# Performance work log

Measured on AMD Instinct MI355X. Metric: run time of the kernel, lower is better.

Reference implementation:

```python
import jax, jax.numpy as jnp
import numpy as np

PAD = 0  # padding_idx


def setup_inputs() -> dict:
    key = jax.random.key(0)
    ks = jax.random.split(key, 10)
    T, B, V, E, H = 64, 32, 32000, 512, 512
    s = 0.05
    tokens = jax.random.randint(ks[0], (T, B), 0, V).astype(jnp.int32)
    emb = jax.random.normal(ks[1], (V, E), jnp.float32) * s
    emb = emb.at[PAD].set(0.0)  # padding_idx row zeroed like nn.Embedding
    return {
        "tokens": tokens,
        "emb": emb,
        "W_ih": jax.random.normal(ks[2], (4 * H, E), jnp.float32) * s,
        "W_hh": jax.random.normal(ks[3], (4 * H, H), jnp.float32) * s,
        "b_ih": jax.random.normal(ks[4], (4 * H,), jnp.float32) * s,
        "b_hh": jax.random.normal(ks[5], (4 * H,), jnp.float32) * s,
        "W_fc": jax.random.normal(ks[6], (V, H), jnp.float32) * s,
        "b_fc": jax.random.normal(ks[7], (V,), jnp.float32) * s,
        "h0": jax.random.normal(ks[8], (B, H), jnp.float32) * s,
        "c0": jax.random.normal(ks[9], (B, H), jnp.float32) * s,
    }


def reference(tokens, emb, W_ih, W_hh, b_ih, b_hh, W_fc, b_fc, h0, c0):
    H = h0.shape[1]

    def step(carry, tok):
        h, c = carry                      # [B,H] each
        x = emb[tok]                      # [B,E] per-token embedding lookup
        gates = x @ W_ih.T + h @ W_hh.T + b_ih + b_hh  # [B,4H]
        i, f, g, o = jnp.split(gates, 4, axis=-1)
        i = jax.nn.sigmoid(i)
        f = jax.nn.sigmoid(f)
        g = jnp.tanh(g)
        o = jax.nn.sigmoid(o)
        c_tmp = f * c + i * g             # LSTMCell cell update
        h_tmp = o * jnp.tanh(c_tmp)
        mask = (tok != PAD)[:, None]      # masked state update: carry state only for non-pad tokens
        h_new = jnp.where(mask, h_tmp, h)
        c_new = jnp.where(mask, c_tmp, c)
        logits = h_tmp @ W_fc.T + b_fc    # [B,V] projection of the tentative hidden (as in source)
        return (h_new, c_new), logits

    (_, _), out = jax.lax.scan(step, (h0, c0), tokens)  # out: [T,B,V]
    return out
```

## Files before the change

### kernel.cpp

```cpp
#include <hip/hip_runtime.h>
#include <stdint.h>

#define TT 64
#define BB 32
#define VV 32000
#define EE 512
#define HH 512
#define G4 2048
#define NBLK 64

typedef float f32x4 __attribute__((ext_vector_type(4)));
typedef short bf16x8 __attribute__((ext_vector_type(8)));

__device__ __forceinline__ unsigned int f2bf(float f) {
    union { float f; uint32_t u; } v; v.f = f;
    uint32_t r = v.u + 0x7fffu + ((v.u >> 16) & 1u);
    return (r >> 16);
}

__global__ __launch_bounds__(256)
void prep_kernel(const float* __restrict__ emb, const int* __restrict__ tokens,
                 const float* __restrict__ h0,
                 unsigned short* __restrict__ Xbf, unsigned short* __restrict__ hb0,
                 unsigned int* __restrict__ syncp) {
    const int NX = TT * BB * EE / 4;
    const int NH = BB * HH / 4;
    int i = blockIdx.x * 256 + threadIdx.x;
    if (i == 0) { syncp[0] = 0u; }
    if (i < NX) {
        int rrow = i >> 7;
        int e4 = i & 127;
        int tok = tokens[rrow];
        float4 v = ((const float4*)(emb + (size_t)tok * EE))[e4];
        uint2 o;
        o.x = f2bf(v.x) | (f2bf(v.y) << 16);
        o.y = f2bf(v.z) | (f2bf(v.w) << 16);
        *(uint2*)(Xbf + (size_t)rrow * EE + e4 * 4) = o;
        return;
    }
    i -= NX;
    if (i < NH) {
        float4 v = ((const float4*)h0)[i];
        uint2 o;
        o.x = f2bf(v.x) | (f2bf(v.y) << 16);
        o.y = f2bf(v.z) | (f2bf(v.w) << 16);
        *(uint2*)(hb0 + i * 4) = o;
    }
}

#define LDA 68

__global__ __launch_bounds__(256, 2)
void gemm_bt(const unsigned short* __restrict__ A, const float* __restrict__ Bm,
             float* __restrict__ Cout, const float* __restrict__ bias1,
             const float* __restrict__ bias2, int N, int K) {
    __shared__ unsigned short lA[128 * LDA];
    __shared__ unsigned short lB[128 * LDA];
    const int tid = threadIdx.x;
    const int lane = tid & 63;
    const int w = tid >> 6;
    const int m0 = blockIdx.y * 128;
    const int n0 = blockIdx.x * 128;
    const int wm = (w & 1) * 64;
    const int wn = (w >> 1) * 64;
    f32x4 acc[4][4];
#pragma unroll
    for (int i = 0; i < 4; ++i)
#pragma unroll
        for (int j = 0; j < 4; ++j) acc[i][j] = (f32x4){0.f, 0.f, 0.f, 0.f};

    for (int k0 = 0; k0 < K; k0 += 64) {
#pragma unroll
        for (int i = 0; i < 4; ++i) {
            int c = tid + 256 * i;
            int row = c >> 3;
            int kg = c & 7;
            uint4 va = *(const uint4*)(A + (size_t)(m0 + row) * K + k0 + kg * 8);
            *(uint2*)&lA[row * LDA + kg * 8]     = make_uint2(va.x, va.y);
            *(uint2*)&lA[row * LDA + kg * 8 + 4] = make_uint2(va.z, va.w);
            const float4* bp = (const float4*)(Bm + (size_t)(n0 + row) * K + k0 + kg * 8);
            float4 b0 = bp[0], b1 = bp[1];
            uint2 p0, p1;
            p0.x = f2bf(b0.x) | (f2bf(b0.y) << 16);
            p0.y = f2bf(b0.z) | (f2bf(b0.w) << 16);
            p1.x = f2bf(b1.x) | (f2bf(b1.y) << 16);
            p1.y = f2bf(b1.z) | (f2bf(b1.w) << 16);
            *(uint2*)&lB[row * LDA + kg * 8]     = p0;
            *(uint2*)&lB[row * LDA + kg * 8 + 4] = p1;
        }
        __syncthreads();
#pragma unroll
        for (int ks = 0; ks < 2; ++ks) {
            const int kgrp = ks * 4 + (lane >> 4);
            bf16x8 af[4], bfr[4];
#pragma unroll
            for (int mi = 0; mi < 4; ++mi) {
                int row = wm + mi * 16 + (lane & 15);
                union { uint2 d[2]; bf16x8 v; } u;
                u.d[0] = *(const uint2*)&lA[row * LDA + kgrp * 8];
                u.d[1] = *(const uint2*)&lA[row * LDA + kgrp * 8 + 4];
                af[mi] = u.v;
            }
#pragma unroll
            for (int ni = 0; ni < 4; ++ni) {
                int row = wn + ni * 16 + (lane & 15);
                union { uint2 d[2]; bf16x8 v; } u;
                u.d[0] = *(const uint2*)&lB[row * LDA + kgrp * 8];
                u.d[1] = *(const uint2*)&lB[row * LDA + kgrp * 8 + 4];
                bfr[ni] = u.v;
            }
#pragma unroll
            for (int mi = 0; mi < 4; ++mi)
#pragma unroll
                for (int ni = 0; ni < 4; ++ni)
                    acc[mi][ni] = __builtin_amdgcn_mfma_f32_16x16x32_bf16(
                        af[mi], bfr[ni], acc[mi][ni], 0, 0, 0);
        }
        __syncthreads();
    }
    const int col_l = lane & 15;
    const int row_l = (lane >> 4) * 4;
#pragma unroll
    for (int ni = 0; ni < 4; ++ni) {
        int col = n0 + wn + ni * 16 + col_l;
        float bv = bias1[col];
        if (bias2) bv += bias2[col];
#pragma unroll
        for (int mi = 0; mi < 4; ++mi) {
            int rowb = m0 + wm + mi * 16 + row_l;
#pragma unroll
            for (int rr = 0; rr < 4; ++rr) {
                Cout[(size_t)(rowb + rr) * N + col] = acc[mi][ni][rr] + bv;
            }
        }
    }
}

__global__ __launch_bounds__(256, 1)
void rec_kernel(const float* __restrict__ XG, const float* __restrict__ Whh,
                const int* __restrict__ tokens, const float* __restrict__ h0,
                const float* __restrict__ c0, unsigned short* __restrict__ hb0,
                unsigned short* __restrict__ hb1, unsigned short* __restrict__ Htmp,
                unsigned int* __restrict__ syncp) {
    __shared__ int ltok[TT * BB];
    const int tid = threadIdx.x;
    const int l = tid & 63;
    const int w = tid >> 6;
    const int mi = w >> 1;
    const int ni = w & 1;
    const int blk = blockIdx.x;

    for (int u = tid; u < TT * BB; u += 256) ltok[u] = tokens[u];

    const int b  = ni * 16 + (l & 15);
    const int hc = mi * 4 + (l >> 4);
    const int jh = blk * 8 + hc;

    const int r = mi * 16 + (l & 15);
    const int hcr = r >> 2;
    const int gr = r & 3;
    const int ksub = (l >> 4) * 8;
    const float* wrow = Whh + ((size_t)gr * HH + (size_t)blk * 8 + hcr) * HH;
    bf16x8 af[16];
#pragma unroll
    for (int kc = 0; kc < 16; ++kc) {
        float4 w0 = *(const float4*)(wrow + kc * 32 + ksub);
        float4 w1 = *(const float4*)(wrow + kc * 32 + ksub + 4);
        union { unsigned short s[8]; bf16x8 v; } u;
        u.s[0] = (unsigned short)f2bf(w0.x);
        u.s[1] = (unsigned short)f2bf(w0.y);
        u.s[2] = (unsigned short)f2bf(w0.z);
        u.s[3] = (unsigned short)f2bf(w0.w);
        u.s[4] = (unsigned short)f2bf(w1.x);
        u.s[5] = (unsigned short)f2bf(w1.y);
        u.s[6] = (unsigned short)f2bf(w1.z);
        u.s[7] = (unsigned short)f2bf(w1.w);
        af[kc] = u.v;
    }

    float hprev = h0[(size_t)b * HH + jh];
    float cprev = c0[(size_t)b * HH + jh];
    __syncthreads();

    for (int t = 0; t < TT; ++t) {
        const unsigned short* hin = (t & 1) ? hb1 : hb0;
        unsigned short* hout = (t & 1) ? hb0 : hb1;

        const float* xg = XG + ((size_t)t * BB + b) * G4 + jh;
        float x0 = xg[0];
        float x1 = xg[HH];
        float x2 = xg[2 * HH];
        float x3 = xg[3 * HH];

        const unsigned short* hrow = hin + (size_t)b * HH + ksub;
        f32x4 acc = {0.f, 0.f, 0.f, 0.f};
#pragma unroll
        for (int kc = 0; kc < 16; ++kc) {
            bf16x8 bfv = *(const bf16x8*)(hrow + kc * 32);
            acc = __builtin_amdgcn_mfma_f32_16x16x32_bf16(af[kc], bfv, acc, 0, 0, 0);
        }

        float gi = acc[0] + x0;
        float gf = acc[1] + x1;
        float gg = acc[2] + x2;
        float go = acc[3] + x3;
        float ig = 1.f / (1.f + __expf(-gi));
        float fg = 1.f / (1.f + __expf(-gf));
        float gt = tanhf(gg);
        float og = 1.f / (1.f + __expf(-go));
        float c_tmp = fg * cprev + ig * gt;
        float h_tmp = og * tanhf(c_tmp);
        const bool msk = ltok[t * BB + b] != 0;
        cprev = msk ? c_tmp : cprev;
        hprev = msk ? h_tmp : hprev;

        Htmp[((size_t)t * BB + b) * HH + jh] = (unsigned short)f2bf(h_tmp);
        hout[(size_t)b * HH + jh] = (unsigned short)f2bf(hprev);

        if (t < TT - 1) {
            __syncthreads();
            if (tid == 0) {
                __hip_atomic_fetch_add(syncp, 1u, __ATOMIC_RELEASE,
                                       __HIP_MEMORY_SCOPE_AGENT);
                const unsigned int tgt = (unsigned int)(t + 1) * NBLK;
                while (__hip_atomic_load(syncp, __ATOMIC_RELAXED,
                                         __HIP_MEMORY_SCOPE_AGENT) < tgt) {
                    __builtin_amdgcn_s_sleep(2);
                }
                (void)__hip_atomic_load(syncp, __ATOMIC_ACQUIRE,
                                        __HIP_MEMORY_SCOPE_AGENT);
            }
            __syncthreads();
        }
    }
}

extern "C" void kernel_launch(void* const* d_in, const int* in_sizes, int n_in,
                              void* d_out, int out_size, void* d_ws, size_t ws_size,
                              hipStream_t stream) {
    const int*   tokens = (const int*)d_in[0];
    const float* emb    = (const float*)d_in[1];
    const float* W_ih   = (const float*)d_in[2];
    const float* W_hh   = (const float*)d_in[3];
    const float* b_ih   = (const float*)d_in[4];
    const float* b_hh   = (const float*)d_in[5];
    const float* W_fc   = (const float*)d_in[6];
    const float* b_fc   = (const float*)d_in[7];
    const float* h0     = (const float*)d_in[8];
    const float* c0     = (const float*)d_in[9];

    char* ws = (char*)d_ws;
    size_t o = 0;
    unsigned short* Xbf  = (unsigned short*)(ws + o); o += (size_t)TT * BB * EE * 2;
    unsigned short* Htmp = (unsigned short*)(ws + o); o += (size_t)TT * BB * HH * 2;
    float* XG = (float*)(ws + o); o += (size_t)TT * BB * G4 * 4;
    unsigned short* hb0 = (unsigned short*)(ws + o); o += (size_t)BB * HH * 2;
    unsigned short* hb1 = (unsigned short*)(ws + o); o += (size_t)BB * HH * 2;
    unsigned int* syncp = (unsigned int*)(ws + o); o += 64;
    (void)ws_size; (void)in_sizes; (void)n_in; (void)out_size;

    prep_kernel<<<1040, 256, 0, stream>>>(emb, tokens, h0, Xbf, hb0, syncp);
    dim3 gx(G4 / 128, (TT * BB) / 128);
    gemm_bt<<<gx, 256, 0, stream>>>(Xbf, W_ih, XG, b_ih, b_hh, G4, EE);
    rec_kernel<<<NBLK, 256, 0, stream>>>(XG, W_hh, tokens, h0, c0, hb0, hb1,
                                         Htmp, syncp);
    dim3 gp(VV / 128, (TT * BB) / 128);
    gemm_bt<<<gp, 256, 0, stream>>>(Htmp, W_fc, (float*)d_out, b_fc, nullptr, VV, HH);
}
```

Measured before the change: 947.8 us.

## Pre-convert weights to bf16, use LDS DMA loads, flag barrier, interleaved gate layout

Weight conversion to bf16 for W_ih and W_fc moves into the prep kernel, so the GEMM can stage A and B tiles straight into LDS with global_load_lds instead of converting in the inner loop. GEMM blocks are remapped with an XCD-aware swizzle. The input-gate GEMM writes its output with the four gates interleaved, so the recurrence reads one float4 per step and prefetches the next step's value. The single atomic-counter grid barrier becomes a flag-and-broadcast barrier coordinated by block 0. The cost is an extra bf16 copy of the 32000x512 W_fc and an unpadded LDS layout that may cause bank conflicts.

```diff
diff --git a/kernel.cpp b/kernel.cpp
--- a/kernel.cpp
+++ b/kernel.cpp
@@ -17,50 +17,80 @@
     uint32_t r = v.u + 0x7fffu + ((v.u >> 16) & 1u);
     return (r >> 16);
 }
+__device__ __forceinline__ uint2 pack4(float4 v) {
+    uint2 o;
+    o.x = f2bf(v.x) | (f2bf(v.y) << 16);
+    o.y = f2bf(v.z) | (f2bf(v.w) << 16);
+    return o;
+}
+
+__device__ __forceinline__ void gload16(const unsigned short* g, unsigned short* l) {
+    __builtin_amdgcn_global_load_lds(
+        (const __attribute__((address_space(1))) unsigned int*)g,
+        (__attribute__((address_space(3))) unsigned int*)l, 16, 0, 0);
+}
 
 __global__ __launch_bounds__(256)
 void prep_kernel(const float* __restrict__ emb, const int* __restrict__ tokens,
-                 const float* __restrict__ h0,
+                 const float* __restrict__ h0, const float* __restrict__ Wih,
+                 const float* __restrict__ Wfc,
                  unsigned short* __restrict__ Xbf, unsigned short* __restrict__ hb0,
+                 unsigned short* __restrict__ Wib, unsigned short* __restrict__ Wfb,
                  unsigned int* __restrict__ syncp) {
     const int NX = TT * BB * EE / 4;
     const int NH = BB * HH / 4;
-    int i = blockIdx.x * 256 + threadIdx.x;
-    if (i == 0) { syncp[0] = 0u; }
-    if (i < NX) {
-        int rrow = i >> 7;
-        int e4 = i & 127;
-        int tok = tokens[rrow];
-        float4 v = ((const float4*)(emb + (size_t)tok * EE))[e4];
-        uint2 o;
-        o.x = f2bf(v.x) | (f2bf(v.y) << 16);
-        o.y = f2bf(v.z) | (f2bf(v.w) << 16);
-        *(uint2*)(Xbf + (size_t)rrow * EE + e4 * 4) = o;
-        return;
-    }
-    i -= NX;
-    if (i < NH) {
-        float4 v = ((const float4*)h0)[i];
-        uint2 o;
-        o.x = f2bf(v.x) | (f2bf(v.y) << 16);
-        o.y = f2bf(v.z) | (f2bf(v.w) << 16);
-        *(uint2*)(hb0 + i * 4) = o;
-    }
-}
-
-#define LDA 68
+    const int NWI = G4 * EE / 4;
+    const int NWF = VV * HH / 4;
+    const int NS = NBLK * 16 + 16;
+    const long total = (long)NX + NH + NWI + NWF + NS;
+    for (long idx = (long)blockIdx.x * 256 + threadIdx.x; idx < total;
+         idx += (long)gridDim.x * 256) {
+        long i = idx;
+        if (i < NX) {
+            int rrow = (int)(i >> 7);
+            int e4 = (int)(i & 127);
+            int tok = tokens[rrow];
+            float4 v = ((const float4*)(emb + (size_t)tok * EE))[e4];
+            *(uint2*)(Xbf + (size_t)rrow * EE + e4 * 4) = pack4(v);
+            continue;
+        }
+        i -= NX;
+        if (i < NH) {
+            float4 v = ((const float4*)h0)[i];
+            *(uint2*)(hb0 + i * 4) = pack4(v);
+            continue;
+        }
+        i -= NH;
+        if (i < NWI) {
+            float4 v = ((const float4*)Wih)[i];
+            *(uint2*)(Wib + i * 4) = pack4(v);
+            continue;
+        }
+        i -= NWI;
+        if (i < NWF) {
+            float4 v = ((const float4*)Wfc)[i];
+            *(uint2*)(Wfb + i * 4) = pack4(v);
+            continue;
+        }
+        i -= NWF;
+        syncp[i] = 0u;
+    }
+}
 
 __global__ __launch_bounds__(256, 2)
-void gemm_bt(const unsigned short* __restrict__ A, const float* __restrict__ Bm,
+void gemm_bb(const unsigned short* __restrict__ A, const unsigned short* __restrict__ B,
              float* __restrict__ Cout, const float* __restrict__ bias1,
-             const float* __restrict__ bias2, int N, int K) {
-    __shared__ unsigned short lA[128 * LDA];
-    __shared__ unsigned short lB[128 * LDA];
+             const float* __restrict__ bias2, int N, int K, int ntn, int mode) {
+    __shared__ unsigned short lA[128 * 64];
+    __shared__ unsigned short lB[128 * 64];
     const int tid = threadIdx.x;
     const int lane = tid & 63;
     const int w = tid >> 6;
-    const int m0 = blockIdx.y * 128;
-    const int n0 = blockIdx.x * 128;
+    const int nwg = gridDim.x;
+    const int cpx = nwg >> 3;
+    const int wid = (blockIdx.x & 7) * cpx + (blockIdx.x >> 3);
+    const int m0 = (wid / ntn) * 128;
+    const int n0 = (wid % ntn) * 128;
     const int wm = (w & 1) * 64;
     const int wn = (w >> 1) * 64;
     f32x4 acc[4][4];
@@ -72,21 +102,11 @@
     for (int k0 = 0; k0 < K; k0 += 64) {
 #pragma unroll
         for (int i = 0; i < 4; ++i) {
-            int c = tid + 256 * i;
+            int c = i * 256 + tid;
             int row = c >> 3;
             int kg = c & 7;
-            uint4 va = *(const uint4*)(A + (size_t)(m0 + row) * K + k0 + kg * 8);
-            *(uint2*)&lA[row * LDA + kg * 8]     = make_uint2(va.x, va.y);
-            *(uint2*)&lA[row * LDA + kg * 8 + 4] = make_uint2(va.z, va.w);
-            const float4* bp = (const float4*)(Bm + (size_t)(n0 + row) * K + k0 + kg * 8);
-            float4 b0 = bp[0], b1 = bp[1];
-            uint2 p0, p1;
-            p0.x = f2bf(b0.x) | (f2bf(b0.y) << 16);
-            p0.y = f2bf(b0.z) | (f2bf(b0.w) << 16);
-            p1.x = f2bf(b1.x) | (f2bf(b1.y) << 16);
-            p1.y = f2bf(b1.z) | (f2bf(b1.w) << 16);
-            *(uint2*)&lB[row * LDA + kg * 8]     = p0;
-            *(uint2*)&lB[row * LDA + kg * 8 + 4] = p1;
+            gload16(A + (size_t)(m0 + row) * K + k0 + kg * 8, &lA[c * 8]);
+            gload16(B + (size_t)(n0 + row) * K + k0 + kg * 8, &lB[c * 8]);
         }
         __syncthreads();
 #pragma unroll
@@ -96,18 +116,12 @@
 #pragma unroll
             for (int mi = 0; mi < 4; ++mi) {
                 int row = wm + mi * 16 + (lane & 15);
-                union { uint2 d[2]; bf16x8 v; } u;
-                u.d[0] = *(const uint2*)&lA[row * LDA + kgrp * 8];
-                u.d[1] = *(const uint2*)&lA[row * LDA + kgrp * 8 + 4];
-                af[mi] = u.v;
+                af[mi] = *(const bf16x8*)&lA[row * 64 + kgrp * 8];
             }
 #pragma unroll
             for (int ni = 0; ni < 4; ++ni) {
                 int row = wn + ni * 16 + (lane & 15);
-                union { uint2 d[2]; bf16x8 v; } u;
-                u.d[0] = *(const uint2*)&lB[row * LDA + kgrp * 8];
-                u.d[1] = *(const uint2*)&lB[row * LDA + kgrp * 8 + 4];
-                bfr[ni] = u.v;
+                bfr[ni] = *(const bf16x8*)&lB[row * 64 + kgrp * 8];
             }
 #pragma unroll
             for (int mi = 0; mi < 4; ++mi)
@@ -130,14 +144,20 @@
             int rowb = m0 + wm + mi * 16 + row_l;
 #pragma unroll
             for (int rr = 0; rr < 4; ++rr) {
-                Cout[(size_t)(rowb + rr) * N + col] = acc[mi][ni][rr] + bv;
+                size_t idx;
+                if (mode) {
+                    idx = (size_t)(rowb + rr) * N + ((col & 511) << 2) + (col >> 9);
+                } else {
+                    idx = (size_t)(rowb + rr) * N + col;
+                }
+                Cout[idx] = acc[mi][ni][rr] + bv;
             }
         }
     }
 }
 
 __global__ __launch_bounds__(256, 1)
-void rec_kernel(const float* __restrict__ XG, const float* __restrict__ Whh,
+void rec_kernel(const float* __restrict__ XG4, const float* __restrict__ Whh,
                 const int* __restrict__ tokens, const float* __restrict__ h0,
                 const float* __restrict__ c0, unsigned short* __restrict__ hb0,
                 unsigned short* __restrict__ hb1, unsigned short* __restrict__ Htmp,
@@ -149,6 +169,8 @@
     const int mi = w >> 1;
     const int ni = w & 1;
     const int blk = blockIdx.x;
+    unsigned int* flags = syncp;
+    unsigned int* go = syncp + NBLK * 16;
 
     for (int u = tid; u < TT * BB; u += 256) ltok[u] = tokens[u];
 
@@ -180,18 +202,15 @@
 
     float hprev = h0[(size_t)b * HH + jh];
     float cprev = c0[(size_t)b * HH + jh];
+
+    const float* xgp = XG4 + (size_t)b * G4 + (size_t)jh * 4;
+    float4 xv = *(const float4*)xgp;
     __syncthreads();
 
     for (int t = 0; t < TT; ++t) {
         const unsigned short* hin = (t & 1) ? hb1 : hb0;
         unsigned short* hout = (t & 1) ? hb0 : hb1;
 
-        const float* xg = XG + ((size_t)t * BB + b) * G4 + jh;
-        float x0 = xg[0];
-        float x1 = xg[HH];
-        float x2 = xg[2 * HH];
-        float x3 = xg[3 * HH];
-
         const unsigned short* hrow = hin + (size_t)b * HH + ksub;
         f32x4 acc = {0.f, 0.f, 0.f, 0.f};
 #pragma unroll
@@ -200,14 +219,14 @@
             acc = __builtin_amdgcn_mfma_f32_16x16x32_bf16(af[kc], bfv, acc, 0, 0, 0);
         }
 
-        float gi = acc[0] + x0;
-        float gf = acc[1] + x1;
-        float gg = acc[2] + x2;
-        float go = acc[3] + x3;
+        float gi = acc[0] + xv.x;
+        float gf = acc[1] + xv.y;
+        float gg = acc[2] + xv.z;
+        float go_ = acc[3] + xv.w;
         float ig = 1.f / (1.f + __expf(-gi));
         float fg = 1.f / (1.f + __expf(-gf));
         float gt = tanhf(gg);
-        float og = 1.f / (1.f + __expf(-go));
+        float og = 1.f / (1.f + __expf(-go_));
         float c_tmp = fg * cprev + ig * gt;
         float h_tmp = og * tanhf(c_tmp);
         const bool msk = ltok[t * BB + b] != 0;
@@ -218,19 +237,32 @@
         hout[(size_t)b * HH + jh] = (unsigned short)f2bf(hprev);
 
         if (t < TT - 1) {
+            float4 xn = *(const float4*)(xgp + (size_t)(t + 1) * BB * G4);
             __syncthreads();
-            if (tid == 0) {
-                __hip_atomic_fetch_add(syncp, 1u, __ATOMIC_RELEASE,
+            if (blk == 0) {
+                if (tid > 0 && tid < NBLK) {
+                    while (__hip_atomic_load(&flags[tid * 16], __ATOMIC_RELAXED,
+                                             __HIP_MEMORY_SCOPE_AGENT) <= (unsigned)t)
+                        __builtin_amdgcn_s_sleep(1);
+                }
+                __syncthreads();
+                if (tid == 0) {
+                    __builtin_amdgcn_fence(__ATOMIC_ACQUIRE, "agent");
+                    __hip_atomic_store(go, (unsigned)(t + 1), __ATOMIC_RELEASE,
                                        __HIP_MEMORY_SCOPE_AGENT);
-                const unsigned int tgt = (unsigned int)(t + 1) * NBLK;
-                while (__hip_atomic_load(syncp, __ATOMIC_RELAXED,
-                                         __HIP_MEMORY_SCOPE_AGENT) < tgt) {
-                    __builtin_amdgcn_s_sleep(2);
                 }
-                (void)__hip_atomic_load(syncp, __ATOMIC_ACQUIRE,
-                                        __HIP_MEMORY_SCOPE_AGENT);
+            } else {
+                if (tid == 0) {
+                    __hip_atomic_store(&flags[blk * 16], (unsigned)(t + 1),
+                                       __ATOMIC_RELEASE, __HIP_MEMORY_SCOPE_AGENT);
+                    while (__hip_atomic_load(go, __ATOMIC_RELAXED,
+                                             __HIP_MEMORY_SCOPE_AGENT) <= (unsigned)t)
+                        __builtin_amdgcn_s_sleep(1);
+                    __builtin_amdgcn_fence(__ATOMIC_ACQUIRE, "agent");
+                }
             }
             __syncthreads();
+            xv = xn;
         }
     }
 }
@@ -254,16 +286,19 @@
     unsigned short* Xbf  = (unsigned short*)(ws + o); o += (size_t)TT * BB * EE * 2;
     unsigned short* Htmp = (unsigned short*)(ws + o); o += (size_t)TT * BB * HH * 2;
     float* XG = (float*)(ws + o); o += (size_t)TT * BB * G4 * 4;
+    unsigned short* Wib = (unsigned short*)(ws + o); o += (size_t)G4 * EE * 2;
+    unsigned short* Wfb = (unsigned short*)(ws + o); o += (size_t)VV * HH * 2;
     unsigned short* hb0 = (unsigned short*)(ws + o); o += (size_t)BB * HH * 2;
     unsigned short* hb1 = (unsigned short*)(ws + o); o += (size_t)BB * HH * 2;
-    unsigned int* syncp = (unsigned int*)(ws + o); o += 64;
+    unsigned int* syncp = (unsigned int*)(ws + o); o += (NBLK * 16 + 16) * 4;
     (void)ws_size; (void)in_sizes; (void)n_in; (void)out_size;
 
-    prep_kernel<<<1040, 256, 0, stream>>>(emb, tokens, h0, Xbf, hb0, syncp);
-    dim3 gx(G4 / 128, (TT * BB) / 128);
-    gemm_bt<<<gx, 256, 0, stream>>>(Xbf, W_ih, XG, b_ih, b_hh, G4, EE);
+    prep_kernel<<<2048, 256, 0, stream>>>(emb, tokens, h0, W_ih, W_fc,
+                                          Xbf, hb0, Wib, Wfb, syncp);
+    gemm_bb<<<(G4 / 128) * ((TT * BB) / 128), 256, 0, stream>>>(
+        Xbf, Wib, XG, b_ih, b_hh, G4, EE, G4 / 128, 1);
     rec_kernel<<<NBLK, 256, 0, stream>>>(XG, W_hh, tokens, h0, c0, hb0, hb1,
                                          Htmp, syncp);
-    dim3 gp(VV / 128, (TT * BB) / 128);
-    gemm_bt<<<gp, 256, 0, stream>>>(Htmp, W_fc, (float*)d_out, b_fc, nullptr, VV, HH);
-}
+    gemm_bb<<<(VV / 128) * ((TT * BB) / 128), 256, 0, stream>>>(
+        Htmp, Wfb, (float*)d_out, b_fc, nullptr, VV, HH, VV / 128, 0);
+}
```

After: 875.5 us. 1.08x faster.
